# Kernel optimization log

Hardware: AMD Instinct MI355X
Metric: run time of the kernel (lower is better)

## Reference

```python
import jax, jax.numpy as jnp
from jax import lax
import numpy as np

S, B, I, H = 1024, 512, 5, 32
G = 4 * H  # torch LSTM gate dim, order: i, f, g, o


def setup_inputs() -> dict:
    key = jax.random.key(0)
    ks = jax.random.split(key, 19)
    n = lambda k, shape, s=0.1: jax.random.normal(k, shape, jnp.float32) * s
    return {
        "x": jax.random.normal(ks[0], (S, B, I), jnp.float32),
        "Wih0": n(ks[1], (G, I)), "Whh0": n(ks[2], (G, H)), "bih0": n(ks[3], (G,)), "bhh0": n(ks[4], (G,)),
        "Wih1": n(ks[5], (G, H)), "Whh1": n(ks[6], (G, H)), "bih1": n(ks[7], (G,)), "bhh1": n(ks[8], (G,)),
        "Wih2": n(ks[9], (G, H)), "Whh2": n(ks[10], (G, H)), "bih2": n(ks[11], (G,)), "bhh2": n(ks[12], (G,)),
        "w1": n(ks[13], (H, H)), "b1": n(ks[14], (H,)),
        "w2": n(ks[15], (H, H)), "b2": n(ks[16], (H,)),
        "w3": n(ks[17], (1, H)), "b3": n(ks[18], (1,)),
    }


def lstm_layer(x, Wih, Whh, bih, bhh):
    # x: [S, B, in]; precompute input projections for all steps (one big GEMM)
    xp = jnp.einsum("sbi,gi->sbg", x, Wih) + bih + bhh  # [S, B, 4H]
    h0 = jnp.zeros((x.shape[1], H), x.dtype)
    c0 = jnp.zeros((x.shape[1], H), x.dtype)

    def step(carry, xg):
        h, c = carry
        gates = xg + h @ Whh.T  # [B, 4H]
        i, f, g, o = jnp.split(gates, 4, axis=-1)
        c = jax.nn.sigmoid(f) * c + jax.nn.sigmoid(i) * jnp.tanh(g)
        h = jax.nn.sigmoid(o) * jnp.tanh(c)
        return (h, c), h

    _, ys = lax.scan(step, (h0, c0), xp)
    return ys  # [S, B, H]


def reference(x, Wih0, Whh0, bih0, bhh0, Wih1, Whh1, bih1, bhh1,
              Wih2, Whh2, bih2, bhh2, w1, b1, w2, b2, w3, b3):
    h = lstm_layer(x, Wih0, Whh0, bih0, bhh0)
    h = lstm_layer(h, Wih1, Whh1, bih1, bhh1)
    h = lstm_layer(h, Wih2, Whh2, bih2, bhh2)  # [S, B, H]
    s, b, hd = h.shape
    y = h.reshape(s * b, hd)
    y = y @ w1.T + b1
    y = y @ w2.T + b2
    y = y @ w3.T + b3
    y = jax.nn.relu(y)
    return y.reshape(s, b, -1)  # [S, B, 1]
```

## Files before the change

kernel.cpp:

```cpp
#include <hip/hip_runtime.h>
#include <math.h>

#define S_LEN 1024
#define BATCH 512
#define HID   32

__device__ __forceinline__ float fast_rcp(float x) { return __builtin_amdgcn_rcpf(x); }

__device__ __forceinline__ float sigmoid_f(float x) {
    return fast_rcp(1.0f + __expf(-x));
}

__device__ __forceinline__ float tanh_f(float x) {
    float t = __expf(-2.0f * fabsf(x));
    float r = (1.0f - t) * fast_rcp(1.0f + t);
    return copysignf(r, x);
}

__device__ __forceinline__ float rl(float v, int k) {
    return __int_as_float(__builtin_amdgcn_readlane(__float_as_int(v), k));
}

__global__ __launch_bounds__(192, 2)
void lstm3_head(const float* __restrict__ x,
                const float* __restrict__ Wih0, const float* __restrict__ Whh0,
                const float* __restrict__ bih0, const float* __restrict__ bhh0,
                const float* __restrict__ Wih1, const float* __restrict__ Whh1,
                const float* __restrict__ bih1, const float* __restrict__ bhh1,
                const float* __restrict__ Wih2, const float* __restrict__ Whh2,
                const float* __restrict__ bih2, const float* __restrict__ bhh2,
                const float* __restrict__ w1, const float* __restrict__ b1,
                const float* __restrict__ w2, const float* __restrict__ b2,
                const float* __restrict__ w3, const float* __restrict__ b3,
                float* __restrict__ out)
{
    const int b = blockIdx.x;
    const int w = threadIdx.x >> 6;
    const int l = threadIdx.x & 63;
    const int j = l & 31;
    const bool lowHalf = (l < 32);
    const int gA = l;
    const int gB = l + 64;

    __shared__ float ring[2][2][HID];
    for (int i = threadIdx.x; i < 2 * 2 * HID; i += 192)
        (&ring[0][0][0])[i] = 0.0f;

    const float* Wih = (w == 0) ? Wih0 : (w == 1) ? Wih1 : Wih2;
    const float* Whh = (w == 0) ? Whh0 : (w == 1) ? Whh1 : Whh2;
    const float* bih = (w == 0) ? bih0 : (w == 1) ? bih1 : bih2;
    const float* bhh = (w == 0) ? bhh0 : (w == 1) ? bhh1 : bhh2;

    float whhA[HID], whhB[HID];
#pragma unroll
    for (int k = 0; k < HID; ++k) {
        whhA[k] = Whh[gA * HID + k];
        whhB[k] = Whh[gB * HID + k];
    }
    float wihA[HID], wihB[HID];
    if (w == 0) {
#pragma unroll
        for (int k = 0; k < 5; ++k) {
            wihA[k] = Wih[gA * 5 + k];
            wihB[k] = Wih[gB * 5 + k];
        }
    } else {
#pragma unroll
        for (int k = 0; k < HID; ++k) {
            wihA[k] = Wih[gA * HID + k];
            wihB[k] = Wih[gB * HID + k];
        }
    }
    const float biasA = bih[gA] + bhh[gA];
    const float biasB = bih[gB] + bhh[gB];

    float u_own = 0.0f, beta = 0.0f;
    if (w == 2) {
        float t_own = 0.0f;
#pragma unroll
        for (int k = 0; k < HID; ++k)
            t_own += w3[k] * w2[k * HID + j];
        float uo = 0.0f, bt = 0.0f;
#pragma unroll
        for (int k = 0; k < HID; ++k) {
            float tk = rl(t_own, k);
            uo += tk * w1[k * HID + j];
            bt += tk * b1[k] + w3[k] * b2[k];
        }
        u_own = uo;
        beta = bt + b3[0];
    }

    float c = 0.0f;
    float h = 0.0f;

    const float* xb = x + (size_t)b * 5;
    float xv0 = 0.f, xv1 = 0.f, xv2 = 0.f, xv3 = 0.f, xv4 = 0.f;
    if (w == 0) { xv0 = xb[0]; xv1 = xb[1]; xv2 = xb[2]; xv3 = xb[3]; xv4 = xb[4]; }

    __syncthreads();

    for (int t = 0; t < S_LEN + 2; ++t) {
        const int s = t - w;
        const bool active = ((unsigned)s < S_LEN);
        const int p = t & 1;

        float4 hin[HID / 4];
        if (w > 0) {
            const float4* r4 = reinterpret_cast<const float4*>(&ring[p][w - 1][0]);
#pragma unroll
            for (int k4 = 0; k4 < HID / 4; ++k4) hin[k4] = r4[k4];
        }

        float aA0 = biasA, aA1 = 0.f, aA2 = 0.f, aA3 = 0.f;
        float aB0 = biasB, aB1 = 0.f, aB2 = 0.f, aB3 = 0.f;
#pragma unroll
        for (int k = 0; k < HID; k += 4) {
            float h0 = rl(h, k + 0);
            float h1 = rl(h, k + 1);
            float h2 = rl(h, k + 2);
            float h3 = rl(h, k + 3);
            aA0 += whhA[k + 0] * h0;  aB0 += whhB[k + 0] * h0;
            aA1 += whhA[k + 1] * h1;  aB1 += whhB[k + 1] * h1;
            aA2 += whhA[k + 2] * h2;  aB2 += whhB[k + 2] * h2;
            aA3 += whhA[k + 3] * h3;  aB3 += whhB[k + 3] * h3;
        }

        if (w == 0) {
            aA0 += wihA[0] * xv0;  aB0 += wihB[0] * xv0;
            aA1 += wihA[1] * xv1;  aB1 += wihB[1] * xv1;
            aA2 += wihA[2] * xv2;  aB2 += wihB[2] * xv2;
            aA3 += wihA[3] * xv3;  aB3 += wihB[3] * xv3;
            aA0 += wihA[4] * xv4;  aB0 += wihB[4] * xv4;
            if (s + 1 < S_LEN) {
                const float* xn = xb + (size_t)(s + 1) * BATCH * 5;
                xv0 = xn[0]; xv1 = xn[1]; xv2 = xn[2]; xv3 = xn[3]; xv4 = xn[4];
            }
        } else {
#pragma unroll
            for (int k4 = 0; k4 < HID / 4; ++k4) {
                float4 hv = hin[k4];
                aA0 += wihA[4 * k4 + 0] * hv.x;  aB0 += wihB[4 * k4 + 0] * hv.x;
                aA1 += wihA[4 * k4 + 1] * hv.y;  aB1 += wihB[4 * k4 + 1] * hv.y;
                aA2 += wihA[4 * k4 + 2] * hv.z;  aB2 += wihB[4 * k4 + 2] * hv.z;
                aA3 += wihA[4 * k4 + 3] * hv.w;  aB3 += wihB[4 * k4 + 3] * hv.w;
            }
        }
        float accA = (aA0 + aA1) + (aA2 + aA3);
        float accB = (aB0 + aB1) + (aB2 + aB3);

        float pA = __shfl_xor(accA, 32);
        float pB = __shfl_xor(accB, 32);
        float gi = lowHalf ? accA : pA;
        float gf = lowHalf ? pA : accA;
        float gg = lowHalf ? accB : pB;
        float go = lowHalf ? pB : accB;

        gi = sigmoid_f(gi);
        gf = sigmoid_f(gf);
        gg = tanh_f(gg);
        go = sigmoid_f(go);
        float c_new = gf * c + gi * gg;
        float h_new = go * tanh_f(c_new);

        if (active) {
            c = c_new;
            h = h_new;
            if (w < 2) {
                if (lowHalf) ring[p ^ 1][w][j] = h_new;
            } else {
                float prt = u_own * h_new;
                prt += __shfl_xor(prt, 1);
                prt += __shfl_xor(prt, 2);
                prt += __shfl_xor(prt, 4);
                prt += __shfl_xor(prt, 8);
                prt += __shfl_xor(prt, 16);
                if (l == 0) out[(size_t)s * BATCH + b] = fmaxf(prt + beta, 0.0f);
            }
        }
        __syncthreads();
    }
}

extern "C" void kernel_launch(void* const* d_in, const int* in_sizes, int n_in,
                              void* d_out, int out_size, void* d_ws, size_t ws_size,
                              hipStream_t stream)
{
    const float* x    = (const float*)d_in[0];
    const float* Wih0 = (const float*)d_in[1];
    const float* Whh0 = (const float*)d_in[2];
    const float* bih0 = (const float*)d_in[3];
    const float* bhh0 = (const float*)d_in[4];
    const float* Wih1 = (const float*)d_in[5];
    const float* Whh1 = (const float*)d_in[6];
    const float* bih1 = (const float*)d_in[7];
    const float* bhh1 = (const float*)d_in[8];
    const float* Wih2 = (const float*)d_in[9];
    const float* Whh2 = (const float*)d_in[10];
    const float* bih2 = (const float*)d_in[11];
    const float* bhh2 = (const float*)d_in[12];
    const float* w1   = (const float*)d_in[13];
    const float* b1   = (const float*)d_in[14];
    const float* w2   = (const float*)d_in[15];
    const float* b2   = (const float*)d_in[16];
    const float* w3   = (const float*)d_in[17];
    const float* b3   = (const float*)d_in[18];

    lstm3_head<<<BATCH, 192, 0, stream>>>(x, Wih0, Whh0, bih0, bhh0,
                                          Wih1, Whh1, bih1, bhh1,
                                          Wih2, Whh2, bih2, bhh2,
                                          w1, b1, w2, b2, w3, b3,
                                          (float*)d_out);
}
```

Baseline: 956.0 us.

## Preload x into LDS and compute recurrent matvec before the barrier

Each block now copies its whole x sequence (1024x5 floats, 20KB) into shared memory up front, so layer 0 no longer issues a global load every step. The recurrent Whh·h product for the next step is moved to just before __syncthreads, so it overlaps with barrier waiting and only the input-projection part runs after the ring buffer is read. In exchange, the added 20KB of LDS per block may reduce occupancy, and a strided prologue load is added.

```diff
diff --git a/kernel.cpp b/kernel.cpp
--- a/kernel.cpp
+++ b/kernel.cpp
@@ -42,7 +42,17 @@
     const int gA = l;
     const int gB = l + 64;
 
+    __shared__ float xlds[S_LEN * 5];
     __shared__ float ring[2][2][HID];
+
+    {
+        const float* xb = x + (size_t)b * 5;
+        for (int i = threadIdx.x; i < S_LEN * 5; i += 192) {
+            int s = i / 5;
+            int k = i - 5 * s;
+            xlds[i] = xb[(size_t)s * (BATCH * 5) + k];
+        }
+    }
     for (int i = threadIdx.x; i < 2 * 2 * HID; i += 192)
         (&ring[0][0][0])[i] = 0.0f;
 
@@ -94,9 +104,8 @@
     float c = 0.0f;
     float h = 0.0f;
 
-    const float* xb = x + (size_t)b * 5;
-    float xv0 = 0.f, xv1 = 0.f, xv2 = 0.f, xv3 = 0.f, xv4 = 0.f;
-    if (w == 0) { xv0 = xb[0]; xv1 = xb[1]; xv2 = xb[2]; xv3 = xb[3]; xv4 = xb[4]; }
+    float aA0 = biasA, aA1 = 0.f, aA2 = 0.f, aA3 = 0.f;
+    float aB0 = biasB, aB1 = 0.f, aB2 = 0.f, aB3 = 0.f;
 
     __syncthreads();
 
@@ -105,49 +114,32 @@
         const bool active = ((unsigned)s < S_LEN);
         const int p = t & 1;
 
-        float4 hin[HID / 4];
-        if (w > 0) {
-            const float4* r4 = reinterpret_cast<const float4*>(&ring[p][w - 1][0]);
-#pragma unroll
-            for (int k4 = 0; k4 < HID / 4; ++k4) hin[k4] = r4[k4];
-        }
-
-        float aA0 = biasA, aA1 = 0.f, aA2 = 0.f, aA3 = 0.f;
-        float aB0 = biasB, aB1 = 0.f, aB2 = 0.f, aB3 = 0.f;
-#pragma unroll
-        for (int k = 0; k < HID; k += 4) {
-            float h0 = rl(h, k + 0);
-            float h1 = rl(h, k + 1);
-            float h2 = rl(h, k + 2);
-            float h3 = rl(h, k + 3);
-            aA0 += whhA[k + 0] * h0;  aB0 += whhB[k + 0] * h0;
-            aA1 += whhA[k + 1] * h1;  aB1 += whhB[k + 1] * h1;
-            aA2 += whhA[k + 2] * h2;  aB2 += whhB[k + 2] * h2;
-            aA3 += whhA[k + 3] * h3;  aB3 += whhB[k + 3] * h3;
-        }
+        float iA0 = 0.f, iA1 = 0.f, iA2 = 0.f, iA3 = 0.f;
+        float iB0 = 0.f, iB1 = 0.f, iB2 = 0.f, iB3 = 0.f;
 
         if (w == 0) {
-            aA0 += wihA[0] * xv0;  aB0 += wihB[0] * xv0;
-            aA1 += wihA[1] * xv1;  aB1 += wihB[1] * xv1;
-            aA2 += wihA[2] * xv2;  aB2 += wihB[2] * xv2;
-            aA3 += wihA[3] * xv3;  aB3 += wihB[3] * xv3;
-            aA0 += wihA[4] * xv4;  aB0 += wihB[4] * xv4;
-            if (s + 1 < S_LEN) {
-                const float* xn = xb + (size_t)(s + 1) * BATCH * 5;
-                xv0 = xn[0]; xv1 = xn[1]; xv2 = xn[2]; xv3 = xn[3]; xv4 = xn[4];
+            if (active) {
+                const float* xs = &xlds[s * 5];
+                float x0 = xs[0], x1 = xs[1], x2 = xs[2], x3 = xs[3], x4 = xs[4];
+                iA0 = wihA[0] * x0 + wihA[4] * x4;
+                iB0 = wihB[0] * x0 + wihB[4] * x4;
+                iA1 = wihA[1] * x1;  iB1 = wihB[1] * x1;
+                iA2 = wihA[2] * x2;  iB2 = wihB[2] * x2;
+                iA3 = wihA[3] * x3;  iB3 = wihB[3] * x3;
             }
         } else {
+            const float4* r4 = reinterpret_cast<const float4*>(&ring[p][w - 1][0]);
 #pragma unroll
             for (int k4 = 0; k4 < HID / 4; ++k4) {
-                float4 hv = hin[k4];
-                aA0 += wihA[4 * k4 + 0] * hv.x;  aB0 += wihB[4 * k4 + 0] * hv.x;
-                aA1 += wihA[4 * k4 + 1] * hv.y;  aB1 += wihB[4 * k4 + 1] * hv.y;
-                aA2 += wihA[4 * k4 + 2] * hv.z;  aB2 += wihB[4 * k4 + 2] * hv.z;
-                aA3 += wihA[4 * k4 + 3] * hv.w;  aB3 += wihB[4 * k4 + 3] * hv.w;
+                float4 hv = r4[k4];
+                iA0 += wihA[4 * k4 + 0] * hv.x;  iB0 += wihB[4 * k4 + 0] * hv.x;
+                iA1 += wihA[4 * k4 + 1] * hv.y;  iB1 += wihB[4 * k4 + 1] * hv.y;
+                iA2 += wihA[4 * k4 + 2] * hv.z;  iB2 += wihB[4 * k4 + 2] * hv.z;
+                iA3 += wihA[4 * k4 + 3] * hv.w;  iB3 += wihB[4 * k4 + 3] * hv.w;
             }
         }
-        float accA = (aA0 + aA1) + (aA2 + aA3);
-        float accB = (aB0 + aB1) + (aB2 + aB3);
+        float accA = ((aA0 + iA0) + (aA1 + iA1)) + ((aA2 + iA2) + (aA3 + iA3));
+        float accB = ((aB0 + iB0) + (aB1 + iB1)) + ((aB2 + iB2) + (aB3 + iB3));
 
         float pA = __shfl_xor(accA, 32);
         float pB = __shfl_xor(accB, 32);
@@ -178,6 +170,21 @@
                 if (l == 0) out[(size_t)s * BATCH + b] = fmaxf(prt + beta, 0.0f);
             }
         }
+
+        aA0 = biasA; aA1 = 0.f; aA2 = 0.f; aA3 = 0.f;
+        aB0 = biasB; aB1 = 0.f; aB2 = 0.f; aB3 = 0.f;
+#pragma unroll
+        for (int k = 0; k < HID; k += 4) {
+            float h0 = rl(h, k + 0);
+            float h1 = rl(h, k + 1);
+            float h2 = rl(h, k + 2);
+            float h3 = rl(h, k + 3);
+            aA0 += whhA[k + 0] * h0;  aB0 += whhB[k + 0] * h0;
+            aA1 += whhA[k + 1] * h1;  aB1 += whhB[k + 1] * h1;
+            aA2 += whhA[k + 2] * h2;  aB2 += whhB[k + 2] * h2;
+            aA3 += whhA[k + 3] * h3;  aB3 += whhB[k + 3] * h3;
+        }
+
         __syncthreads();
     }
 }
```

Result: slower. 1.143 ms (+19.6%).
